# Kernel optimization log

Measured on AMD Instinct MI355X. Metric: run time of the kernel, lower is better.

The kernel has to match this reference:

```python
import jax, jax.numpy as jnp
import numpy as np

D_MODEL = 1024
N_HEADS = 16
DEPTH = D_MODEL // N_HEADS
D_FF = 4096
B, S = 2, 2048
EPS = 1e-5


def _layernorm(x, g, b):
    mu = jnp.mean(x, axis=-1, keepdims=True)
    var = jnp.mean(jnp.square(x - mu), axis=-1, keepdims=True)
    return (x - mu) * jax.lax.rsqrt(var + EPS) * g + b


def setup_inputs() -> dict:
    key = jax.random.key(0)
    ks = jax.random.split(key, 16)
    sd = 0.02
    d = {
        'x': jax.random.normal(ks[0], (B, S, D_MODEL), dtype=jnp.float32),
        'mask': jnp.ones((B, S), dtype=jnp.int32),
        'wq_w': jax.random.normal(ks[1], (D_MODEL, D_MODEL), dtype=jnp.float32) * sd,
        'wq_b': jnp.zeros((D_MODEL,), dtype=jnp.float32),
        'wk_w': jax.random.normal(ks[2], (D_MODEL, D_MODEL), dtype=jnp.float32) * sd,
        'wk_b': jnp.zeros((D_MODEL,), dtype=jnp.float32),
        'wv_w': jax.random.normal(ks[3], (D_MODEL, D_MODEL), dtype=jnp.float32) * sd,
        'wv_b': jnp.zeros((D_MODEL,), dtype=jnp.float32),
        'wo_w': jax.random.normal(ks[4], (D_MODEL, D_MODEL), dtype=jnp.float32) * sd,
        'wo_b': jnp.zeros((D_MODEL,), dtype=jnp.float32),
        'ffn_w1': jax.random.normal(ks[5], (D_MODEL, D_FF), dtype=jnp.float32) * sd,
        'ffn_b1': jnp.zeros((D_FF,), dtype=jnp.float32),
        'ffn_w2': jax.random.normal(ks[6], (D_FF, D_MODEL), dtype=jnp.float32) * sd,
        'ffn_b2': jnp.zeros((D_MODEL,), dtype=jnp.float32),
        'ln1_g': jnp.ones((D_MODEL,), dtype=jnp.float32),
        'ln1_b': jnp.zeros((D_MODEL,), dtype=jnp.float32),
        'ln2_g': jnp.ones((D_MODEL,), dtype=jnp.float32),
        'ln2_b': jnp.zeros((D_MODEL,), dtype=jnp.float32),
    }
    return d


def reference(x, mask, wq_w, wq_b, wk_w, wk_b, wv_w, wv_b, wo_w, wo_b,
              ffn_w1, ffn_b1, ffn_w2, ffn_b2, ln1_g, ln1_b, ln2_g, ln2_b):
    b, s, _ = x.shape
    # projections [B,S,D] -> [B,H,S,depth]
    def split_heads(t):
        return t.reshape(b, s, N_HEADS, DEPTH).transpose(0, 2, 1, 3)
    q = split_heads(x @ wq_w + wq_b)
    k = split_heads(x @ wk_w + wk_b)
    v = split_heads(x @ wv_w + wv_b)
    # scores [B,H,S,S]
    logits = jnp.einsum('bhqd,bhkd->bhqk', q, k) / jnp.sqrt(jnp.float32(DEPTH))
    m = mask[:, None, None, :]  # [B,1,1,S] broadcast over heads/query
    logits = jnp.where(m == 0, jnp.float32(-1e9), logits)
    attn = jax.nn.softmax(logits, axis=-1)
    ctx = jnp.einsum('bhqk,bhkd->bhqd', attn, v)
    ctx = ctx.transpose(0, 2, 1, 3).reshape(b, s, D_MODEL)
    attn_out = ctx @ wo_w + wo_b
    out1 = _layernorm(x + attn_out, ln1_g, ln1_b)
    ffn = jax.nn.relu(out1 @ ffn_w1 + ffn_b1) @ ffn_w2 + ffn_b2
    out2 = _layernorm(out1 + ffn, ln2_g, ln2_b)
    return out2
```

## Files before the change

### kernel.cpp

```cpp
#include <hip/hip_runtime.h>
#include <hip/hip_bf16.h>

#define D_MODEL 1024
#define N_HEADS 16
#define DEPTH   64
#define D_FF    4096
#define BATCH   2
#define SEQ     2048
#define NTOK    (BATCH * SEQ)
#define EPS     1e-5f

typedef __attribute__((ext_vector_type(8))) short short8;
typedef __attribute__((ext_vector_type(4))) float f32x4;
typedef __attribute__((ext_vector_type(4))) unsigned short ushort4v;
typedef __attribute__((ext_vector_type(8))) unsigned short ushort8v;

__device__ __forceinline__ unsigned short f2bf(float f) {
    union { __hip_bfloat16 h; unsigned short u; } cv;
    cv.h = __float2bfloat16(f);
    return cv.u;
}

__device__ __forceinline__ float exp2_fast(float x) {
    float r;
    asm("v_exp_f32 %0, %1" : "=v"(r) : "v"(x));
    return r;
}

__device__ __forceinline__ void gload16(const unsigned short* g, unsigned short* lds) {
    __builtin_amdgcn_global_load_lds(
        (const __attribute__((address_space(1))) void*)g,
        (__attribute__((address_space(3))) void*)lds, 16, 0, 0);
}

__global__ __launch_bounds__(256) void cast_bf16_kernel(
    const float* __restrict__ in, unsigned short* __restrict__ out, int n)
{
    int i = (blockIdx.x * 256 + threadIdx.x) * 8;
    if (i >= n) return;
    f32x4 a = *(const f32x4*)&in[i];
    f32x4 b = *(const f32x4*)&in[i + 4];
    ushort8v o;
    o[0] = f2bf(a[0]); o[1] = f2bf(a[1]); o[2] = f2bf(a[2]); o[3] = f2bf(a[3]);
    o[4] = f2bf(b[0]); o[5] = f2bf(b[1]); o[6] = f2bf(b[2]); o[7] = f2bf(b[3]);
    *(ushort8v*)&out[i] = o;
}

__global__ __launch_bounds__(256) void transpose_cast_kernel(
    const float* __restrict__ W, unsigned short* __restrict__ WT, int K, int N)
{
    __shared__ float t[64][65];
    const int bk = blockIdx.y * 64, bn = blockIdx.x * 64;
    const int c4 = threadIdx.x & 15, r0 = threadIdx.x >> 4;
#pragma unroll
    for (int i = 0; i < 4; ++i) {
        int k = r0 + i * 16;
        f32x4 v = *(const f32x4*)&W[(size_t)(bk + k) * N + bn + c4 * 4];
#pragma unroll
        for (int jj = 0; jj < 4; ++jj) t[k][c4 * 4 + jj] = v[jj];
    }
    __syncthreads();
#pragma unroll
    for (int i = 0; i < 4; ++i) {
        int n = r0 + i * 16;
        ushort4v o;
#pragma unroll
        for (int jj = 0; jj < 4; ++jj) o[jj] = f2bf(t[c4 * 4 + jj][n]);
        *(ushort4v*)&WT[(size_t)(bn + n) * K + bk + c4 * 4] = o;
    }
}

__global__ __launch_bounds__(256) void concat3_kernel(
    const float* __restrict__ a, const float* __restrict__ b,
    const float* __restrict__ c, float* __restrict__ o)
{
    int i = blockIdx.x * 256 + threadIdx.x;
    if (i < 1024) o[i] = a[i];
    else if (i < 2048) o[i] = b[i - 1024];
    else if (i < 3072) o[i] = c[i - 2048];
}

__global__ __launch_bounds__(256) void vtrans_kernel(
    const unsigned short* __restrict__ QKV, unsigned short* __restrict__ Vt)
{
    __shared__ unsigned short T[64][72];
    const int st = blockIdx.x * 64;
    const int h = blockIdx.y, b = blockIdx.z;
    const int tid = threadIdx.x;
    const size_t tok0 = (size_t)b * SEQ;
    const int LD = 3 * D_MODEL;
    const int r = tid >> 3, c8 = (tid & 7) * 8;
#pragma unroll
    for (int p = 0; p < 2; ++p) {
        int row = p * 32 + r;
        *(ushort8v*)&T[row][c8] =
            *(const ushort8v*)&QKV[(tok0 + st + row) * LD + 2048 + h * 64 + c8];
    }
    __syncthreads();
    const int bh = b * N_HEADS + h;
#pragma unroll
    for (int p = 0; p < 2; ++p) {
        int d = p * 32 + r;
        ushort8v o;
#pragma unroll
        for (int e = 0; e < 8; ++e) o[e] = T[c8 + e][d];
        *(ushort8v*)&Vt[((size_t)bh * 64 + d) * SEQ + st + c8] = o;
    }
}

__global__ __launch_bounds__(512, 2) void gemm256_kernel(
    const unsigned short* __restrict__ A, const unsigned short* __restrict__ BT,
    const float* __restrict__ bias, float* __restrict__ C,
    unsigned short* __restrict__ Cb,
    int M, int N, int lda, int kLen, int ksplit, int relu, int out_bf)
{
    __shared__ unsigned short As[2][256 * 64];
    __shared__ unsigned short Bs[2][256 * 64];
    const int tid = threadIdx.x;
    const int lane = tid & 63, w = tid >> 6;
    const int wr = w >> 2, wc = w & 3;
    const int lr = lane & 15, g = lane >> 4;

    const int nwg = gridDim.x;
    int wg = blockIdx.x;
    if ((nwg & 7) == 0) wg = (wg & 7) * (nwg >> 3) + (wg >> 3);
    if (ksplit > 1) {
        const int ntile = nwg / ksplit;
        const int split = wg / ntile;
        wg = wg % ntile;
        A  += (size_t)split * kLen;
        BT += (size_t)split * kLen;
        C  += (size_t)split * M * N;
    }
    const int gx = N >> 8;
    const int bm = (wg / gx) * 256, bn = (wg % gx) * 256;

    const int srow = (w << 3) + (lane >> 3);
    const int scol = ((lane & 7) ^ (lane >> 3)) << 3;
    const int ldst = (w << 9);

#define STG(P, Xs, bufi, hf, rb, k0)                                            \
    {                                                                            \
        gload16(P + (size_t)((rb) + (hf) * 128 + srow) * lda + (k0) + scol,      \
                &Xs[bufi][(hf) * 8192 + ldst]);                                  \
        gload16(P + (size_t)((rb) + (hf) * 128 + 64 + srow) * lda + (k0) + scol, \
                &Xs[bufi][(hf) * 8192 + 4096 + ldst]);                           \
    }

    const int NS = kLen >> 6;
    f32x4 acc[8][4] = {};

    STG(A,  As, 0, 0, bm, 0); STG(A,  As, 0, 1, bm, 0);
    STG(BT, Bs, 0, 0, bn, 0); STG(BT, Bs, 0, 1, bn, 0);
    if (NS > 1) { STG(BT, Bs, 1, 0, bn, 64); STG(BT, Bs, 1, 1, bn, 64); }
    asm volatile("s_waitcnt vmcnt(4)" ::: "memory");
    __builtin_amdgcn_s_barrier();
    asm volatile("" ::: "memory");

    int buf = 0;
    short8 af[4][2], b0[2][2], b1[2][2];
    for (int s = 0; s < NS; ++s) {
        const int kn1 = (s + 1) << 6, kn2 = (s + 2) << 6;

#pragma unroll
        for (int i = 0; i < 4; ++i)
#pragma unroll
            for (int kk = 0; kk < 2; ++kk)
                af[i][kk] = *(const short8*)&As[buf][(wr * 128 + i * 16 + lr) * 64
                                                    + (((kk * 4 + g) ^ (lr & 7)) << 3)];
#pragma unroll
        for (int j = 0; j < 2; ++j)
#pragma unroll
            for (int kk = 0; kk < 2; ++kk)
                b0[j][kk] = *(const short8*)&Bs[buf][(wc * 64 + j * 16 + lr) * 64
                                                    + (((kk * 4 + g) ^ (lr & 7)) << 3)];
        if (s + 1 < NS) STG(A, As, buf ^ 1, 0, bm, kn1);
        asm volatile("" ::: "memory");
        __builtin_amdgcn_s_barrier();
        asm volatile("" ::: "memory");
        __builtin_amdgcn_s_setprio(1);
#pragma unroll
        for (int i = 0; i < 4; ++i)
#pragma unroll
            for (int j = 0; j < 2; ++j) {
                acc[i][j] = __builtin_amdgcn_mfma_f32_16x16x32_bf16(af[i][0], b0[j][0], acc[i][j], 0, 0, 0);
                acc[i][j] = __builtin_amdgcn_mfma_f32_16x16x32_bf16(af[i][1], b0[j][1], acc[i][j], 0, 0, 0);
            }
        __builtin_amdgcn_s_setprio(0);
        asm volatile("" ::: "memory");
        __builtin_amdgcn_s_barrier();
        asm volatile("" ::: "memory");

#pragma unroll
        for (int j = 0; j < 2; ++j)
#pragma unroll
            for (int kk = 0; kk < 2; ++kk)
                b1[j][kk] = *(const short8*)&Bs[buf][(wc * 64 + (j + 2) * 16 + lr) * 64
                                                    + (((kk * 4 + g) ^ (lr & 7)) << 3)];
        if (s + 1 < NS) STG(A, As, buf ^ 1, 1, bm, kn1);
        asm volatile("" ::: "memory");
        __builtin_amdgcn_s_barrier();
        asm volatile("" ::: "memory");
        __builtin_amdgcn_s_setprio(1);
#pragma unroll
        for (int i = 0; i < 4; ++i)
#pragma unroll
            for (int j = 0; j < 2; ++j) {
                acc[i][j + 2] = __builtin_amdgcn_mfma_f32_16x16x32_bf16(af[i][0], b1[j][0], acc[i][j + 2], 0, 0, 0);
                acc[i][j + 2] = __builtin_amdgcn_mfma_f32_16x16x32_bf16(af[i][1], b1[j][1], acc[i][j + 2], 0, 0, 0);
            }
        __builtin_amdgcn_s_setprio(0);
        asm volatile("" ::: "memory");
        __builtin_amdgcn_s_barrier();
        asm volatile("" ::: "memory");

#pragma unroll
        for (int i = 0; i < 4; ++i)
#pragma unroll
            for (int kk = 0; kk < 2; ++kk)
                af[i][kk] = *(const short8*)&As[buf][(wr * 128 + 64 + i * 16 + lr) * 64
                                                    + (((kk * 4 + g) ^ (lr & 7)) << 3)];
        if (s + 2 < NS) STG(BT, Bs, buf, 0, bn, kn2);
        asm volatile("" ::: "memory");
        __builtin_amdgcn_s_barrier();
        asm volatile("" ::: "memory");
        __builtin_amdgcn_s_setprio(1);
#pragma unroll
        for (int i = 0; i < 4; ++i)
#pragma unroll
            for (int j = 0; j < 2; ++j) {
                acc[i + 4][j] = __builtin_amdgcn_mfma_f32_16x16x32_bf16(af[i][0], b0[j][0], acc[i + 4][j], 0, 0, 0);
                acc[i + 4][j] = __builtin_amdgcn_mfma_f32_16x16x32_bf16(af[i][1], b0[j][1], acc[i + 4][j], 0, 0, 0);
            }
        __builtin_amdgcn_s_setprio(0);
        asm volatile("" ::: "memory");
        __builtin_amdgcn_s_barrier();
        asm volatile("" ::: "memory");

        if (s + 2 < NS) STG(BT, Bs, buf, 1, bn, kn2);
        asm volatile("" ::: "memory");
        __builtin_amdgcn_s_barrier();
        asm volatile("" ::: "memory");
        __builtin_amdgcn_s_setprio(1);
#pragma unroll
        for (int i = 0; i < 4; ++i)
#pragma unroll
            for (int j = 0; j < 2; ++j) {
                acc[i + 4][j + 2] = __builtin_amdgcn_mfma_f32_16x16x32_bf16(af[i][0], b1[j][0], acc[i + 4][j + 2], 0, 0, 0);
                acc[i + 4][j + 2] = __builtin_amdgcn_mfma_f32_16x16x32_bf16(af[i][1], b1[j][1], acc[i + 4][j + 2], 0, 0, 0);
            }
        __builtin_amdgcn_s_setprio(0);
        asm volatile("s_waitcnt vmcnt(4)" ::: "memory");
        __builtin_amdgcn_s_barrier();
        asm volatile("" ::: "memory");

        buf ^= 1;
    }
#undef STG

#pragma unroll
    for (int i = 0; i < 8; ++i)
#pragma unroll
        for (int j = 0; j < 4; ++j) {
            const int col = bn + wc * 64 + j * 16 + lr;
            const float bv = bias ? bias[col] : 0.f;
#pragma unroll
            for (int r = 0; r < 4; ++r) {
                const int row = bm + wr * 128 + i * 16 + g * 4 + r;
                float v = acc[i][j][r] + bv;
                if (relu) v = fmaxf(v, 0.f);
                if (out_bf) Cb[(size_t)row * N + col] = f2bf(v);
                else        C [(size_t)row * N + col] = v;
            }
        }
}

__global__ __launch_bounds__(256) void gemm_bt_kernel(
    const unsigned short* __restrict__ A, const unsigned short* __restrict__ BT,
    const float* __restrict__ bias, float* __restrict__ C,
    unsigned short* __restrict__ Cb,
    int M, int N, int lda, int kLen, int relu, int out_bf)
{
    __shared__ unsigned short As[128 * 64];
    __shared__ unsigned short Bs[128 * 64];
    const int tid = threadIdx.x;
    const int lane = tid & 63, wv = tid >> 6;
    const int wr = wv >> 1, wc = wv & 1;
    const int bm = blockIdx.y * 128, bn = blockIdx.x * 128;
    const int kbase = blockIdx.z * kLen;
    const int lr = lane & 15, lk = (lane >> 4) << 3;

    C += (size_t)blockIdx.z * M * N;

    f32x4 acc[4][4] = {};

    for (int kt = 0; kt < kLen; kt += 64) {
#pragma unroll
        for (int c = 0; c < 4; ++c) {
            int e = c * 2048 + tid * 8;
            int row = e >> 6, k = e & 63;
            gload16(A  + (size_t)(bm + row) * lda + kbase + kt + k, As + c * 2048 + wv * 512);
            gload16(BT + (size_t)(bn + row) * lda + kbase + kt + k, Bs + c * 2048 + wv * 512);
        }
        __syncthreads();
#pragma unroll
        for (int kk = 0; kk < 2; ++kk) {
            short8 af[4], bfr[4];
#pragma unroll
            for (int i = 0; i < 4; ++i) {
                af[i]  = *(const short8*)&As[(wr * 64 + i * 16 + lr) * 64 + kk * 32 + lk];
                bfr[i] = *(const short8*)&Bs[(wc * 64 + i * 16 + lr) * 64 + kk * 32 + lk];
            }
#pragma unroll
            for (int i = 0; i < 4; ++i)
#pragma unroll
                for (int j = 0; j < 4; ++j)
                    acc[i][j] = __builtin_amdgcn_mfma_f32_16x16x32_bf16(
                        af[i], bfr[j], acc[i][j], 0, 0, 0);
        }
        __syncthreads();
    }

    const int r0 = bm + wr * 64, c0 = bn + wc * 64;
    const int rq = (lane >> 4) * 4;
#pragma unroll
    for (int i = 0; i < 4; ++i)
#pragma unroll
        for (int j = 0; j < 4; ++j) {
            int col = c0 + j * 16 + lr;
            float bv = bias ? bias[col] : 0.f;
#pragma unroll
            for (int r = 0; r < 4; ++r) {
                int row = r0 + i * 16 + rq + r;
                float v = acc[i][j][r] + bv;
                if (relu) v = fmaxf(v, 0.f);
                if (out_bf) Cb[(size_t)row * N + col] = f2bf(v);
                else        C [(size_t)row * N + col] = v;
            }
        }
}

__global__ __launch_bounds__(256, 3) void attn_mfma_kernel(
    const unsigned short* __restrict__ QKV,
    const unsigned short* __restrict__ Vt,
    const int* __restrict__ mask,
    float* __restrict__ Op, float* __restrict__ ml)
{
    const int tid = threadIdx.x;
    const int lane = tid & 63, w = tid >> 6;
    const int lr = lane & 15, g = lane >> 4;
    const int qt = blockIdx.x * 128;
    const int h = blockIdx.y;
    const int b = blockIdx.z >> 1, sp = blockIdx.z & 1;
    const int bh = b * N_HEADS + h;
    const size_t tok0 = (size_t)b * SEQ;
    const int kvb0 = sp * (SEQ / 2);
    const int LD = 3 * D_MODEL;
    const float C1 = 0.18033688f;

    __shared__ unsigned short Ks[2][64 * 64];
    __shared__ unsigned short Vs[2][64 * 64];
    __shared__ unsigned short Ps[4][32 * 64];
    __shared__ float Msk[2][64];

    short8 qf[2][2];
#pragma unroll
    for (int i = 0; i < 2; ++i)
#pragma unroll
        for (int kk = 0; kk < 2; ++kk)
            qf[i][kk] = *(const short8*)&QKV[(tok0 + qt + w * 32 + i * 16 + lr) * LD
                                             + h * 64 + kk * 32 + g * 8];

    const int rsub = w * 8 + (lane >> 3);
    const int slot = lane & 7;

    float m_[2] = {-1e30f, -1e30f}, l_[2] = {0.f, 0.f};
    f32x4 o_[2][4] = {};

    {
#pragma unroll
        for (int p = 0; p < 2; ++p) {
            const int row = p * 32 + rsub;
            const int ss = slot ^ (row & 7);
            gload16(QKV + (tok0 + kvb0 + row) * LD + D_MODEL + h * 64 + ss * 8,
                    &Ks[0][(p * 32 + w * 8) * 64]);
            gload16(Vt + ((size_t)bh * 64 + row) * SEQ + kvb0 + ss * 8,
                    &Vs[0][(p * 32 + w * 8) * 64]);
        }
        if (tid < 64) Msk[0][tid] = mask[b * SEQ + kvb0 + tid] ? 0.f : -1e9f;
    }
    __syncthreads();

    const int NT = (SEQ / 2) / 64;
    int buf = 0;
    for (int t = 0; t < NT; ++t) {
        if (t + 1 < NT) {
            const int nb = buf ^ 1;
            const int kvn = kvb0 + (t + 1) * 64;
#pragma unroll
            for (int p = 0; p < 2; ++p) {
                const int row = p * 32 + rsub;
                const int ss = slot ^ (row & 7);
                gload16(QKV + (tok0 + kvn + row) * LD + D_MODEL + h * 64 + ss * 8,
                        &Ks[nb][(p * 32 + w * 8) * 64]);
                gload16(Vt + ((size_t)bh * 64 + row) * SEQ + kvn + ss * 8,
                        &Vs[nb][(p * 32 + w * 8) * 64]);
            }
            if (tid < 64) Msk[nb][tid] = mask[b * SEQ + kvn + tid] ? 0.f : -1e9f;
        }

        f32x4 sacc[2][4] = {};
#pragma unroll
        for (int j = 0; j < 4; ++j) {
            short8 kf0 = *(const short8*)&Ks[buf][(j * 16 + lr) * 64 + ((0 + g) ^ (lr & 7)) * 8];
            short8 kf1 = *(const short8*)&Ks[buf][(j * 16 + lr) * 64 + ((4 + g) ^ (lr & 7)) * 8];
#pragma unroll
            for (int i = 0; i < 2; ++i) {
                sacc[i][j] = __builtin_amdgcn_mfma_f32_16x16x32_bf16(kf0, qf[i][0], sacc[i][j], 0, 0, 0);
                sacc[i][j] = __builtin_amdgcn_mfma_f32_16x16x32_bf16(kf1, qf[i][1], sacc[i][j], 0, 0, 0);
            }
        }

        float mb[4][4];
#pragma unroll
        for (int j = 0; j < 4; ++j) {
            f32x4 mrow = *(const f32x4*)&Msk[buf][j * 16 + g * 4];
#pragma unroll
            for (int r = 0; r < 4; ++r) mb[j][r] = mrow[r];
        }

#pragma unroll
        for (int i = 0; i < 2; ++i) {
            float x[4][4];
            float tm = -1e30f;
#pragma unroll
            for (int j = 0; j < 4; ++j)
#pragma unroll
                for (int r = 0; r < 4; ++r) {
                    x[j][r] = fmaf(sacc[i][j][r], C1, mb[j][r]);
                    tm = fmaxf(tm, x[j][r]);
                }
            tm = fmaxf(tm, __shfl_xor(tm, 16));
            tm = fmaxf(tm, __shfl_xor(tm, 32));
            if (__any(tm > m_[i] + 8.f)) {
                const float nm = fmaxf(m_[i], tm);
                const float sc = exp2_fast(m_[i] - nm);
                m_[i] = nm;
                l_[i] *= sc;
#pragma unroll
                for (int r = 0; r < 4; ++r) {
                    const float s_r = __shfl(sc, g * 4 + r);
#pragma unroll
                    for (int dj = 0; dj < 4; ++dj) o_[i][dj][r] *= s_r;
                }
            }
            float rs = 0.f;
#pragma unroll
            for (int j = 0; j < 4; ++j) {
                ushort4v pw;
#pragma unroll
                for (int r = 0; r < 4; ++r) {
                    const float e = exp2_fast(x[j][r] - m_[i]);
                    rs += e;
                    pw[r] = f2bf(e);
                }
                *(ushort4v*)((char*)&Ps[w][0] + (i * 16 + lr) * 128
                             + ((j * 32 + g * 8) ^ ((lr & 7) << 4))) = pw;
            }
            rs += __shfl_xor(rs, 16);
            rs += __shfl_xor(rs, 32);
            l_[i] += rs;
        }

#pragma unroll
        for (int kk = 0; kk < 2; ++kk) {
            short8 pf[2];
#pragma unroll
            for (int i = 0; i < 2; ++i)
                pf[i] = *(const short8*)&Ps[w][(i * 16 + lr) * 64 + ((kk * 4 + g) ^ (lr & 7)) * 8];
#pragma unroll
            for (int dj = 0; dj < 4; ++dj) {
                short8 vf = *(const short8*)&Vs[buf][(dj * 16 + lr) * 64 + ((kk * 4 + g) ^ (lr & 7)) * 8];
#pragma unroll
                for (int i = 0; i < 2; ++i)
                    o_[i][dj] = __builtin_amdgcn_mfma_f32_16x16x32_bf16(pf[i], vf, o_[i][dj], 0, 0, 0);
            }
        }

        __syncthreads();
        buf ^= 1;
    }

    const int rowbase = (sp * 32 + bh) * 2048;
#pragma unroll
    for (int i = 0; i < 2; ++i) {
#pragma unroll
        for (int r = 0; r < 4; ++r) {
            const int q = qt + w * 32 + i * 16 + g * 4 + r;
            float* op = Op + (size_t)(rowbase + q) * 64;
#pragma unroll
            for (int dj = 0; dj < 4; ++dj) op[dj * 16 + lr] = o_[i][dj][r];
        }
        if (g == 0) {
            const int q2 = qt + w * 32 + i * 16 + lr;
            float2 v; v.x = m_[i]; v.y = l_[i];
            ((float2*)ml)[rowbase + q2] = v;
        }
    }
}

__global__ __launch_bounds__(256) void attn_merge_kernel(
    const float* __restrict__ Op, const float* __restrict__ ml,
    unsigned short* __restrict__ ctx)
{
    const int tid = threadIdx.x;
    const int row = blockIdx.x * 16 + (tid >> 4);
    const int d4 = (tid & 15) * 4;
    const int bh = row >> 11, q = row & 2047;
    const int b = bh >> 4, h = bh & 15;
    const float2 v0 = ((const float2*)ml)[row];
    const float2 v1 = ((const float2*)ml)[65536 + row];
    const float m = fmaxf(v0.x, v1.x);
    const float a0 = exp2_fast(v0.x - m), a1 = exp2_fast(v1.x - m);
    const float inv = 1.f / (v0.y * a0 + v1.y * a1);
    f32x4 O0 = *(const f32x4*)&Op[(size_t)row * 64 + d4];
    f32x4 O1 = *(const f32x4*)&Op[((size_t)65536 + row) * 64 + d4];
    ushort4v o;
#pragma unroll
    for (int e = 0; e < 4; ++e)
        o[e] = f2bf((O0[e] * a0 + O1[e] * a1) * inv);
    *(ushort4v*)&ctx[((size_t)(b * SEQ + q)) * D_MODEL + h * 64 + d4] = o;
}

__global__ __launch_bounds__(256) void reduce_ln_kernel(
    const float* __restrict__ P, int nsplit, const float* __restrict__ bias,
    const float* __restrict__ X, const float* __restrict__ g,
    const float* __restrict__ be, float* __restrict__ out,
    unsigned short* __restrict__ outb)
{
    const int row = blockIdx.x, tid = threadIdx.x;
    __shared__ float red[4];
    const size_t MN = (size_t)NTOK * D_MODEL;
    const size_t base = (size_t)row * D_MODEL + tid * 4;

    f32x4 s = *(const f32x4*)(X + base);
    f32x4 bb = *(const f32x4*)(bias + tid * 4);
    s += bb;
    for (int sp = 0; sp < nsplit; ++sp)
        s += *(const f32x4*)(P + sp * MN + base);

    float ls = s[0] + s[1] + s[2] + s[3];
#pragma unroll
    for (int o = 32; o > 0; o >>= 1) ls += __shfl_down(ls, o);
    if ((tid & 63) == 0) red[tid >> 6] = ls;
    __syncthreads();
    const float mu = (red[0] + red[1] + red[2] + red[3]) * (1.f / D_MODEL);
    __syncthreads();

    float d0 = s[0] - mu, d1 = s[1] - mu, d2 = s[2] - mu, d3 = s[3] - mu;
    float lv = d0 * d0 + d1 * d1 + d2 * d2 + d3 * d3;
#pragma unroll
    for (int o = 32; o > 0; o >>= 1) lv += __shfl_down(lv, o);
    if ((tid & 63) == 0) red[tid >> 6] = lv;
    __syncthreads();
    const float var = (red[0] + red[1] + red[2] + red[3]) * (1.f / D_MODEL);
    const float inv = rsqrtf(var + EPS);

    f32x4 gv = *(const f32x4*)(g + tid * 4);
    f32x4 bv = *(const f32x4*)(be + tid * 4);
    f32x4 o4 = {d0 * inv * gv[0] + bv[0], d1 * inv * gv[1] + bv[1],
                d2 * inv * gv[2] + bv[2], d3 * inv * gv[3] + bv[3]};
    *(f32x4*)(out + base) = o4;
    if (outb) {
        ushort4v ob = {f2bf(o4[0]), f2bf(o4[1]), f2bf(o4[2]), f2bf(o4[3])};
        *(ushort4v*)(outb + base) = ob;
    }
}

extern "C" void kernel_launch(void* const* d_in, const int* in_sizes, int n_in,
                              void* d_out, int out_size, void* d_ws, size_t ws_size,
                              hipStream_t stream) {
    const float* x      = (const float*)d_in[0];
    const int*   mask   = (const int*)  d_in[1];
    const float* wq_w   = (const float*)d_in[2];
    const float* wq_b   = (const float*)d_in[3];
    const float* wk_w   = (const float*)d_in[4];
    const float* wk_b   = (const float*)d_in[5];
    const float* wv_w   = (const float*)d_in[6];
    const float* wv_b   = (const float*)d_in[7];
    const float* wo_w   = (const float*)d_in[8];
    const float* wo_b   = (const float*)d_in[9];
    const float* ffn_w1 = (const float*)d_in[10];
    const float* ffn_b1 = (const float*)d_in[11];
    const float* ffn_w2 = (const float*)d_in[12];
    const float* ffn_b2 = (const float*)d_in[13];
    const float* ln1_g  = (const float*)d_in[14];
    const float* ln1_b  = (const float*)d_in[15];
    const float* ln2_g  = (const float*)d_in[16];
    const float* ln2_b  = (const float*)d_in[17];
    float* out = (float*)d_out;

    char* w = (char*)d_ws;
    const size_t MB = 1024 * 1024;
    unsigned short* actb    = (unsigned short*)(w);
    unsigned short* wqkvT   = (unsigned short*)(w + 8 * MB);
    float*          biasqkv = (float*)(w + 14 * MB);
    unsigned short* qkvb    = (unsigned short*)(w + 16 * MB);
    unsigned short* vt      = (unsigned short*)(w + 40 * MB);
    unsigned short* ctxb    = (unsigned short*)(w + 48 * MB);
    float*          Opb     = (float*)(w + 56 * MB);
    float*          mlb     = (float*)(w + 88 * MB);
    float*          woP     = (float*)(w);
    unsigned short* out1b   = (unsigned short*)(w + 40 * MB);
    unsigned short* fhb     = (unsigned short*)(w + 64 * MB);
    unsigned short* w2T     = (unsigned short*)(w + 96 * MB);
    unsigned short* woT     = (unsigned short*)(w + 104 * MB);
    float*          Out1    = (float*)(w + 104 * MB);
    unsigned short* w1T     = (unsigned short*)(w + 120 * MB);
    float*          f2P     = (float*)(w);

    dim3 blk(256);

    transpose_cast_kernel<<<dim3(16, 16), blk, 0, stream>>>(wq_w, wqkvT,               1024, 1024);
    transpose_cast_kernel<<<dim3(16, 16), blk, 0, stream>>>(wk_w, wqkvT + 1024 * 1024, 1024, 1024);
    transpose_cast_kernel<<<dim3(16, 16), blk, 0, stream>>>(wv_w, wqkvT + 2048 * 1024, 1024, 1024);
    transpose_cast_kernel<<<dim3(16, 16), blk, 0, stream>>>(wo_w, woT, 1024, 1024);
    transpose_cast_kernel<<<dim3(64, 16), blk, 0, stream>>>(ffn_w1, w1T, 1024, 4096);
    transpose_cast_kernel<<<dim3(16, 64), blk, 0, stream>>>(ffn_w2, w2T, 4096, 1024);
    concat3_kernel<<<dim3(12), blk, 0, stream>>>(wq_b, wk_b, wv_b, biasqkv);
    cast_bf16_kernel<<<dim3(2048), blk, 0, stream>>>(x, actb, NTOK * D_MODEL);

    gemm256_kernel<<<dim3(192), dim3(512), 0, stream>>>(actb, wqkvT, biasqkv, nullptr, qkvb,
                                                        NTOK, 3072, 1024, 1024, 1, 0, 1);
    vtrans_kernel<<<dim3(SEQ / 64, N_HEADS, BATCH), blk, 0, stream>>>(qkvb, vt);

    attn_mfma_kernel<<<dim3(SEQ / 128, N_HEADS, BATCH * 2), blk, 0, stream>>>(qkvb, vt, mask,
                                                                              Opb, mlb);
    attn_merge_kernel<<<dim3((BATCH * N_HEADS * SEQ) / 16), blk, 0, stream>>>(Opb, mlb, ctxb);

    gemm_bt_kernel<<<dim3(8, 32, 2), blk, 0, stream>>>(ctxb, woT, nullptr, woP, nullptr,
                                                       NTOK, 1024, 1024, 512, 0, 0);
    reduce_ln_kernel<<<dim3(NTOK), blk, 0, stream>>>(woP, 2, wo_b, x, ln1_g, ln1_b,
                                                     Out1, out1b);
    gemm256_kernel<<<dim3(256), dim3(512), 0, stream>>>(out1b, w1T, ffn_b1, nullptr, fhb,
                                                        NTOK, D_FF, 1024, 1024, 1, 1, 1);
    gemm256_kernel<<<dim3(256), dim3(512), 0, stream>>>(fhb, w2T, nullptr, f2P, nullptr,
                                                        NTOK, 1024, 4096, 1024, 4, 0, 0);
    reduce_ln_kernel<<<dim3(NTOK), blk, 0, stream>>>(f2P, 4, ffn_b2, Out1, ln2_g, ln2_b,
                                                     out, nullptr);
}
```

Before: 277.7 us.

## Double attention block to 512 threads covering 256 queries per block

```diff
diff --git a/kernel.cpp b/kernel.cpp
--- a/kernel.cpp
+++ b/kernel.cpp
@@ -340,7 +340,7 @@
         }
 }
 
-__global__ __launch_bounds__(256, 3) void attn_mfma_kernel(
+__global__ __launch_bounds__(512, 4) void attn_mfma_kernel(
     const unsigned short* __restrict__ QKV,
     const unsigned short* __restrict__ Vt,
     const int* __restrict__ mask,
@@ -349,7 +349,7 @@
     const int tid = threadIdx.x;
     const int lane = tid & 63, w = tid >> 6;
     const int lr = lane & 15, g = lane >> 4;
-    const int qt = blockIdx.x * 128;
+    const int qt = blockIdx.x * 256;
     const int h = blockIdx.y;
     const int b = blockIdx.z >> 1, sp = blockIdx.z & 1;
     const int bh = b * N_HEADS + h;
@@ -360,7 +360,7 @@
 
     __shared__ unsigned short Ks[2][64 * 64];
     __shared__ unsigned short Vs[2][64 * 64];
-    __shared__ unsigned short Ps[4][32 * 64];
+    __shared__ unsigned short Ps[8][32 * 64];
     __shared__ float Msk[2][64];
 
     short8 qf[2][2];
@@ -373,20 +373,16 @@
 
     const int rsub = w * 8 + (lane >> 3);
     const int slot = lane & 7;
+    const int sswz = (slot ^ (lane >> 3)) * 8;
 
     float m_[2] = {-1e30f, -1e30f}, l_[2] = {0.f, 0.f};
     f32x4 o_[2][4] = {};
 
     {
-#pragma unroll
-        for (int p = 0; p < 2; ++p) {
-            const int row = p * 32 + rsub;
-            const int ss = slot ^ (row & 7);
-            gload16(QKV + (tok0 + kvb0 + row) * LD + D_MODEL + h * 64 + ss * 8,
-                    &Ks[0][(p * 32 + w * 8) * 64]);
-            gload16(Vt + ((size_t)bh * 64 + row) * SEQ + kvb0 + ss * 8,
-                    &Vs[0][(p * 32 + w * 8) * 64]);
-        }
+        gload16(QKV + (tok0 + kvb0 + rsub) * LD + D_MODEL + h * 64 + sswz,
+                &Ks[0][(w * 8) * 64]);
+        gload16(Vt + ((size_t)bh * 64 + rsub) * SEQ + kvb0 + sswz,
+                &Vs[0][(w * 8) * 64]);
         if (tid < 64) Msk[0][tid] = mask[b * SEQ + kvb0 + tid] ? 0.f : -1e9f;
     }
     __syncthreads();
@@ -397,15 +393,10 @@
         if (t + 1 < NT) {
             const int nb = buf ^ 1;
             const int kvn = kvb0 + (t + 1) * 64;
-#pragma unroll
-            for (int p = 0; p < 2; ++p) {
-                const int row = p * 32 + rsub;
-                const int ss = slot ^ (row & 7);
-                gload16(QKV + (tok0 + kvn + row) * LD + D_MODEL + h * 64 + ss * 8,
-                        &Ks[nb][(p * 32 + w * 8) * 64]);
-                gload16(Vt + ((size_t)bh * 64 + row) * SEQ + kvn + ss * 8,
-                        &Vs[nb][(p * 32 + w * 8) * 64]);
-            }
+            gload16(QKV + (tok0 + kvn + rsub) * LD + D_MODEL + h * 64 + sswz,
+                    &Ks[nb][(w * 8) * 64]);
+            gload16(Vt + ((size_t)bh * 64 + rsub) * SEQ + kvn + sswz,
+                    &Vs[nb][(w * 8) * 64]);
             if (tid < 64) Msk[nb][tid] = mask[b * SEQ + kvn + tid] ? 0.f : -1e9f;
         }
 
@@ -634,8 +625,8 @@
                                                         NTOK, 3072, 1024, 1024, 1, 0, 1);
     vtrans_kernel<<<dim3(SEQ / 64, N_HEADS, BATCH), blk, 0, stream>>>(qkvb, vt);
 
-    attn_mfma_kernel<<<dim3(SEQ / 128, N_HEADS, BATCH * 2), blk, 0, stream>>>(qkvb, vt, mask,
-                                                                              Opb, mlb);
+    attn_mfma_kernel<<<dim3(SEQ / 256, N_HEADS, BATCH * 2), dim3(512), 0, stream>>>(
+        qkvb, vt, mask, Opb, mlb);
     attn_merge_kernel<<<dim3((BATCH * N_HEADS * SEQ) / 16), blk, 0, stream>>>(Opb, mlb, ctxb);
 
     gemm_bt_kernel<<<dim3(8, 32, 2), blk, 0, stream>>>(ctxb, woT, nullptr, woP, nullptr,
```

Result: no change. 281.3 us (+1.3%).

## Compute softmax row sums via MFMA with ones, defer rescale, store partials in bf16

Applied to the files above, without the earlier changes.

```diff
diff --git a/kernel.cpp b/kernel.cpp
--- a/kernel.cpp
+++ b/kernel.cpp
@@ -19,6 +19,12 @@
     union { __hip_bfloat16 h; unsigned short u; } cv;
     cv.h = __float2bfloat16(f);
     return cv.u;
+}
+
+__device__ __forceinline__ float bf2f(unsigned short u) {
+    union { float f; unsigned int i; } c;
+    c.i = (unsigned int)u << 16;
+    return c.f;
 }
 
 __device__ __forceinline__ float exp2_fast(float x) {
@@ -344,7 +350,7 @@
     const unsigned short* __restrict__ QKV,
     const unsigned short* __restrict__ Vt,
     const int* __restrict__ mask,
-    float* __restrict__ Op, float* __restrict__ ml)
+    unsigned short* __restrict__ Op, float* __restrict__ mA, float* __restrict__ lA)
 {
     const int tid = threadIdx.x;
     const int lane = tid & 63, w = tid >> 6;
@@ -363,6 +369,10 @@
     __shared__ unsigned short Ps[4][32 * 64];
     __shared__ float Msk[2][64];
 
+    short8 onesB;
+#pragma unroll
+    for (int e = 0; e < 8; ++e) onesB[e] = (short)0x3F80;
+
     short8 qf[2][2];
 #pragma unroll
     for (int i = 0; i < 2; ++i)
@@ -374,7 +384,8 @@
     const int rsub = w * 8 + (lane >> 3);
     const int slot = lane & 7;
 
-    float m_[2] = {-1e30f, -1e30f}, l_[2] = {0.f, 0.f};
+    float m_[2] = {20.f, 20.f};
+    f32x4 lacc[2] = {};
     f32x4 o_[2][4] = {};
 
     {
@@ -429,6 +440,7 @@
             for (int r = 0; r < 4; ++r) mb[j][r] = mrow[r];
         }
 
+        float tmv[2];
 #pragma unroll
         for (int i = 0; i < 2; ++i) {
             float x[4][4];
@@ -440,51 +452,51 @@
                     x[j][r] = fmaf(sacc[i][j][r], C1, mb[j][r]);
                     tm = fmaxf(tm, x[j][r]);
                 }
+#pragma unroll
+            for (int j = 0; j < 4; ++j) {
+                ushort4v pw;
+#pragma unroll
+                for (int r = 0; r < 4; ++r)
+                    pw[r] = f2bf(exp2_fast(x[j][r] - m_[i]));
+                *(ushort4v*)((char*)&Ps[w][0] + (i * 16 + lr) * 128
+                             + ((j * 32 + g * 8) ^ ((lr & 7) << 4))) = pw;
+            }
             tm = fmaxf(tm, __shfl_xor(tm, 16));
             tm = fmaxf(tm, __shfl_xor(tm, 32));
-            if (__any(tm > m_[i] + 8.f)) {
-                const float nm = fmaxf(m_[i], tm);
+            tmv[i] = tm;
+        }
+
+#pragma unroll
+        for (int kk = 0; kk < 2; ++kk) {
+            short8 pf[2];
+#pragma unroll
+            for (int i = 0; i < 2; ++i) {
+                pf[i] = *(const short8*)&Ps[w][(i * 16 + lr) * 64 + ((kk * 4 + g) ^ (lr & 7)) * 8];
+                lacc[i] = __builtin_amdgcn_mfma_f32_16x16x32_bf16(pf[i], onesB, lacc[i], 0, 0, 0);
+            }
+#pragma unroll
+            for (int dj = 0; dj < 4; ++dj) {
+                short8 vf = *(const short8*)&Vs[buf][(dj * 16 + lr) * 64 + ((kk * 4 + g) ^ (lr & 7)) * 8];
+#pragma unroll
+                for (int i = 0; i < 2; ++i)
+                    o_[i][dj] = __builtin_amdgcn_mfma_f32_16x16x32_bf16(pf[i], vf, o_[i][dj], 0, 0, 0);
+            }
+        }
+
+#pragma unroll
+        for (int i = 0; i < 2; ++i) {
+            if (__any(tmv[i] > m_[i] + 8.f)) {
+                const float nm = fmaxf(m_[i], tmv[i]);
                 const float sc = exp2_fast(m_[i] - nm);
                 m_[i] = nm;
-                l_[i] *= sc;
 #pragma unroll
                 for (int r = 0; r < 4; ++r) {
                     const float s_r = __shfl(sc, g * 4 + r);
+                    lacc[i][r] *= s_r;
 #pragma unroll
                     for (int dj = 0; dj < 4; ++dj) o_[i][dj][r] *= s_r;
                 }
             }
-            float rs = 0.f;
-#pragma unroll
-            for (int j = 0; j < 4; ++j) {
-                ushort4v pw;
-#pragma unroll
-                for (int r = 0; r < 4; ++r) {
-                    const float e = exp2_fast(x[j][r] - m_[i]);
-                    rs += e;
-                    pw[r] = f2bf(e);
-                }
-                *(ushort4v*)((char*)&Ps[w][0] + (i * 16 + lr) * 128
-                             + ((j * 32 + g * 8) ^ ((lr & 7) << 4))) = pw;
-            }
-            rs += __shfl_xor(rs, 16);
-            rs += __shfl_xor(rs, 32);
-            l_[i] += rs;
-        }
-
-#pragma unroll
-        for (int kk = 0; kk < 2; ++kk) {
-            short8 pf[2];
-#pragma unroll
-            for (int i = 0; i < 2; ++i)
-                pf[i] = *(const short8*)&Ps[w][(i * 16 + lr) * 64 + ((kk * 4 + g) ^ (lr & 7)) * 8];
-#pragma unroll
-            for (int dj = 0; dj < 4; ++dj) {
-                short8 vf = *(const short8*)&Vs[buf][(dj * 16 + lr) * 64 + ((kk * 4 + g) ^ (lr & 7)) * 8];
-#pragma unroll
-                for (int i = 0; i < 2; ++i)
-                    o_[i][dj] = __builtin_amdgcn_mfma_f32_16x16x32_bf16(pf[i], vf, o_[i][dj], 0, 0, 0);
-            }
         }
 
         __syncthreads();
@@ -497,38 +509,39 @@
 #pragma unroll
         for (int r = 0; r < 4; ++r) {
             const int q = qt + w * 32 + i * 16 + g * 4 + r;
-            float* op = Op + (size_t)(rowbase + q) * 64;
-#pragma unroll
-            for (int dj = 0; dj < 4; ++dj) op[dj * 16 + lr] = o_[i][dj][r];
-        }
-        if (g == 0) {
-            const int q2 = qt + w * 32 + i * 16 + lr;
-            float2 v; v.x = m_[i]; v.y = l_[i];
-            ((float2*)ml)[rowbase + q2] = v;
+            unsigned short* op = Op + (size_t)(rowbase + q) * 64;
+#pragma unroll
+            for (int dj = 0; dj < 4; ++dj) op[dj * 16 + lr] = f2bf(o_[i][dj][r]);
+        }
+        if (g == 0) mA[rowbase + qt + w * 32 + i * 16 + lr] = m_[i];
+        if (lr == 0) {
+#pragma unroll
+            for (int r = 0; r < 4; ++r)
+                lA[rowbase + qt + w * 32 + i * 16 + g * 4 + r] = lacc[i][r];
         }
     }
 }
 
 __global__ __launch_bounds__(256) void attn_merge_kernel(
-    const float* __restrict__ Op, const float* __restrict__ ml,
-    unsigned short* __restrict__ ctx)
+    const unsigned short* __restrict__ Op, const float* __restrict__ mA,
+    const float* __restrict__ lA, unsigned short* __restrict__ ctx)
 {
     const int tid = threadIdx.x;
     const int row = blockIdx.x * 16 + (tid >> 4);
     const int d4 = (tid & 15) * 4;
     const int bh = row >> 11, q = row & 2047;
     const int b = bh >> 4, h = bh & 15;
-    const float2 v0 = ((const float2*)ml)[row];
-    const float2 v1 = ((const float2*)ml)[65536 + row];
-    const float m = fmaxf(v0.x, v1.x);
-    const float a0 = exp2_fast(v0.x - m), a1 = exp2_fast(v1.x - m);
-    const float inv = 1.f / (v0.y * a0 + v1.y * a1);
-    f32x4 O0 = *(const f32x4*)&Op[(size_t)row * 64 + d4];
-    f32x4 O1 = *(const f32x4*)&Op[((size_t)65536 + row) * 64 + d4];
+    const float m0 = mA[row], m1 = mA[65536 + row];
+    const float l0 = lA[row], l1 = lA[65536 + row];
+    const float m = fmaxf(m0, m1);
+    const float a0 = exp2_fast(m0 - m), a1 = exp2_fast(m1 - m);
+    const float inv = 1.f / (l0 * a0 + l1 * a1);
+    ushort4v O0 = *(const ushort4v*)&Op[(size_t)row * 64 + d4];
+    ushort4v O1 = *(const ushort4v*)&Op[((size_t)65536 + row) * 64 + d4];
     ushort4v o;
 #pragma unroll
     for (int e = 0; e < 4; ++e)
-        o[e] = f2bf((O0[e] * a0 + O1[e] * a1) * inv);
+        o[e] = f2bf((bf2f(O0[e]) * a0 + bf2f(O1[e]) * a1) * inv);
     *(ushort4v*)&ctx[((size_t)(b * SEQ + q)) * D_MODEL + h * 64 + d4] = o;
 }
 
@@ -608,14 +621,15 @@
     unsigned short* qkvb    = (unsigned short*)(w + 16 * MB);
     unsigned short* vt      = (unsigned short*)(w + 40 * MB);
     unsigned short* ctxb    = (unsigned short*)(w + 48 * MB);
-    float*          Opb     = (float*)(w + 56 * MB);
-    float*          mlb     = (float*)(w + 88 * MB);
+    unsigned short* Opb     = (unsigned short*)(w + 56 * MB);
+    float*          mAb     = (float*)(w + 72 * MB);
+    float*          lAb     = (float*)(w + 73 * MB);
+    unsigned short* woT     = (unsigned short*)(w + 74 * MB);
     float*          woP     = (float*)(w);
+    float*          Out1    = (float*)(w + 64 * MB);
     unsigned short* out1b   = (unsigned short*)(w + 40 * MB);
-    unsigned short* fhb     = (unsigned short*)(w + 64 * MB);
-    unsigned short* w2T     = (unsigned short*)(w + 96 * MB);
-    unsigned short* woT     = (unsigned short*)(w + 104 * MB);
-    float*          Out1    = (float*)(w + 104 * MB);
+    unsigned short* fhb     = (unsigned short*)(w + 80 * MB);
+    unsigned short* w2T     = (unsigned short*)(w + 112 * MB);
     unsigned short* w1T     = (unsigned short*)(w + 120 * MB);
     float*          f2P     = (float*)(w);
 
@@ -634,9 +648,10 @@
                                                         NTOK, 3072, 1024, 1024, 1, 0, 1);
     vtrans_kernel<<<dim3(SEQ / 64, N_HEADS, BATCH), blk, 0, stream>>>(qkvb, vt);
 
-    attn_mfma_kernel<<<dim3(SEQ / 128, N_HEADS, BATCH * 2), blk, 0, stream>>>(qkvb, vt, mask,
-                                                                              Opb, mlb);
-    attn_merge_kernel<<<dim3((BATCH * N_HEADS * SEQ) / 16), blk, 0, stream>>>(Opb, mlb, ctxb);
+    attn_mfma_kernel<<<dim3(SEQ / 128, N_HEADS, BATCH * 2), blk, 0, stream>>>(
+        qkvb, vt, mask, Opb, mAb, lAb);
+    attn_merge_kernel<<<dim3((BATCH * N_HEADS * SEQ) / 16), blk, 0, stream>>>(
+        Opb, mAb, lAb, ctxb);
 
     gemm_bt_kernel<<<dim3(8, 32, 2), blk, 0, stream>>>(ctxb, woT, nullptr, woP, nullptr,
                                                        NTOK, 1024, 1024, 512, 0, 0);
```

Result: faster. 270.0 us (-2.8%).
